# Kernel tuning notes

Measured on AMD Instinct MI355X. Metric: run time of the kernel, lower is better.

Reference implementation:

```python
import jax, jax.numpy as jnp
import numpy as np

DISTANCE_SCALE = 25.0
VIEW_PE = 6
STEP = 0.02  # nominal ray-march step size used to scale dists


def positional_encoding(positions, freqs):
    # matches torch: (positions[..., None] * 2**k).reshape(..., freqs*C) -> [sin, cos]
    freq_bands = 2.0 ** jnp.arange(freqs, dtype=positions.dtype)
    pts = (positions[..., None] * freq_bands).reshape(positions.shape[:-1] + (freqs * positions.shape[-1],))
    return jnp.concatenate([jnp.sin(pts), jnp.cos(pts)], axis=-1)


def setup_inputs() -> dict:
    key = jax.random.key(0)
    ks = jax.random.split(key, 10)
    n_rays, n_samples, C, featureC = 4096, 256, 27, 128
    in_mlpC = 3 + 2 * VIEW_PE * 3 + C  # 66
    density_features = jax.random.normal(ks[0], (n_rays, n_samples), jnp.float32)
    app_features = jax.random.normal(ks[1], (n_rays, n_samples, C), jnp.float32)
    viewdirs = jax.random.normal(ks[2], (n_rays, 3), jnp.float32)
    viewdirs = viewdirs / jnp.linalg.norm(viewdirs, axis=-1, keepdims=True)
    dists = jax.random.uniform(ks[3], (n_rays, n_samples), jnp.float32) * STEP
    s1 = 1.0 / np.sqrt(in_mlpC)
    s2 = 1.0 / np.sqrt(featureC)
    W1 = jax.random.uniform(ks[4], (in_mlpC, featureC), jnp.float32, -s1, s1)
    b1 = jax.random.uniform(ks[5], (featureC,), jnp.float32, -s1, s1)
    W2 = jax.random.uniform(ks[6], (featureC, featureC), jnp.float32, -s2, s2)
    b2 = jax.random.uniform(ks[7], (featureC,), jnp.float32, -s2, s2)
    W3 = jax.random.uniform(ks[8], (featureC, 3), jnp.float32, -s2, s2)
    b3 = jnp.zeros((3,), jnp.float32)  # torch init: constant_(bias, 0)
    return {"density_features": density_features, "app_features": app_features,
            "viewdirs": viewdirs, "dists": dists,
            "W1": W1, "b1": b1, "W2": W2, "b2": b2, "W3": W3, "b3": b3}


def reference(density_features, app_features, viewdirs, dists, W1, b1, W2, b2, W3, b3):
    # feature2density (relu activation)
    sigma = jax.nn.relu(density_features)  # [R, S]
    # raw2alpha
    alpha = 1.0 - jnp.exp(-sigma * dists * DISTANCE_SCALE)  # [R, S]
    T = jnp.cumprod(jnp.concatenate([jnp.ones((alpha.shape[0], 1), alpha.dtype),
                                     1.0 - alpha + 1e-10], axis=-1), axis=-1)
    weights = alpha * T[:, :-1]  # [R, S]
    # radiance MLP over all sample points
    R, S, C = app_features.shape
    vd = jnp.broadcast_to(viewdirs[:, None, :], (R, S, 3))
    mlp_in = jnp.concatenate([app_features, vd, positional_encoding(vd, VIEW_PE)], axis=-1)  # [R,S,66]
    h = jax.nn.relu(mlp_in @ W1 + b1)
    h = jax.nn.relu(h @ W2 + b2)
    rgb = jax.nn.sigmoid(h @ W3 + b3)  # [R, S, 3]
    # composite (white background)
    acc_map = jnp.sum(weights, axis=-1)  # [R]
    rgb_map = jnp.einsum('rs,rsc->rc', weights, rgb)  # [R, 3]
    rgb_map = jnp.clip(rgb_map + (1.0 - acc_map[:, None]), 0.0, 1.0)
    return rgb_map
```

## Files before the change

### kernel.cpp

```cpp
#include <hip/hip_runtime.h>
#include <hip/hip_bf16.h>

typedef float f32x4 __attribute__((ext_vector_type(4)));
typedef short s16x8 __attribute__((ext_vector_type(8)));
typedef unsigned int u32;
typedef u32 u32x2 __attribute__((ext_vector_type(2)));

#define DIST_SCALE 25.0f

__device__ __forceinline__ unsigned short f2b(float f) {
  union { float f; unsigned u; } v; v.f = f;
  unsigned r = v.u + 0x7fffu + ((v.u >> 16) & 1u);
  return (unsigned short)(r >> 16);
}

__device__ __forceinline__ u32 cvtpk(float lo, float hi) {
  u32 r;
  asm("v_cvt_pk_bf16_f32 %0, %1, %2" : "=v"(r) : "v"(lo), "v"(hi));
  return r;
}

__device__ __forceinline__ int swzH(int s, int chbyte) {
  return (s * 256 + chbyte) ^ ((s & 7) << 4);
}

__global__ void prep_weights(const float* __restrict__ W1, const float* __restrict__ W2,
                             const float* __restrict__ W3, unsigned short* __restrict__ ws) {
  int t = blockIdx.x * 256 + threadIdx.x;
  int stride = gridDim.x * 256;
  for (int i = t; i < 128 * 32; i += stride) {
    int n = i >> 5, k = i & 31;
    ws[i] = (k < 27) ? f2b(W1[k * 128 + n]) : (unsigned short)0;
  }
  unsigned short* w2t = ws + 4096;
  for (int i = t; i < 128 * 128; i += stride) {
    int n = i >> 7, k = i & 127;
    w2t[i] = f2b(W2[k * 128 + n]);
  }
  unsigned short* w3p = ws + 4096 + 16384;
  for (int i = t; i < 4 * 16 * 32; i += stride) {
    int wv = i >> 9, rem = i & 511, n = rem >> 5, ks = rem & 31;
    int kg = ks >> 3, j = ks & 7;
    int ch = wv * 32 + ((j >> 2) << 4) + kg * 4 + (j & 3);
    w3p[i] = (n < 3) ? f2b(W3[ch * 3 + n]) : (unsigned short)0;
  }
}

__global__ void __launch_bounds__(256, 3) nerf_main(
    const float* __restrict__ dens, const float* __restrict__ app,
    const float* __restrict__ vdirs, const float* __restrict__ dists,
    const float* __restrict__ W1, const float* __restrict__ b1,
    const float* __restrict__ b2v, const float* __restrict__ b3v,
    const unsigned short* __restrict__ wsb, float* __restrict__ out) {
  __shared__ unsigned short HA[64 * 128];
  __shared__ __align__(16) float pool[768];
  __shared__ float wbuf[256];
  __shared__ float red[4][4];

  const int t = threadIdx.x;
  const int lane = t & 63;
  const int wv = t >> 6;
  const int r = blockIdx.x;

  const unsigned short* W1aT = wsb;
  const unsigned short* W2T = wsb + 4096;
  const unsigned short* W3P = wsb + 4096 + 16384;
  char* HAb = (char*)HA;

  const int cl = lane & 15;
  const int kg = lane >> 4;
  const int chBase = wv * 32;
  float* featbuf = pool;
  float* hcbuf = pool + 64;

  if (t < 39) {
    float val;
    if (t < 3) val = vdirs[r * 3 + t];
    else {
      int jj = t - 3;
      int trig = jj / 18;
      int rem = jj % 18;
      int c = rem / 6, k = rem % 6;
      float v = vdirs[r * 3 + c] * (float)(1 << k);
      val = trig ? cosf(v) : sinf(v);
    }
    featbuf[t] = val;
  }
  if (wv == 0) {
    const float4 dv = *(const float4*)(dens + (size_t)r * 256 + lane * 4);
    const float4 tv = *(const float4*)(dists + (size_t)r * 256 + lane * 4);
    float f[4], al[4];
    float dl[4] = {dv.x, dv.y, dv.z, dv.w};
    float tl[4] = {tv.x, tv.y, tv.z, tv.w};
    float p = 1.0f;
#pragma unroll
    for (int q = 0; q < 4; ++q) {
      float sg = fmaxf(dl[q], 0.0f);
      float e = __expf(-sg * tl[q] * DIST_SCALE);
      al[q] = 1.0f - e;
      f[q] = e + 1e-10f;
      p *= f[q];
    }
    float P = p;
#pragma unroll
    for (int dlt = 1; dlt < 64; dlt <<= 1) {
      float v = __shfl_up(P, dlt, 64);
      if (lane >= dlt) P *= v;
    }
    float E = __shfl_up(P, 1, 64);
    if (lane == 0) E = 1.0f;
    float tr = E;
#pragma unroll
    for (int q = 0; q < 4; ++q) { wbuf[lane * 4 + q] = al[q] * tr; tr *= f[q]; }
  }
  __syncthreads();
  if (t < 128) {
    float s = b1[t];
    for (int j = 0; j < 39; ++j) s += featbuf[j] * W1[(27 + j) * 128 + t];
    hcbuf[t] = s;
  }

  s16x8 w1f[2], w2f[2][4], w3s;
#pragma unroll
  for (int nt = 0; nt < 2; ++nt)
    w1f[nt] = *(const s16x8*)(W1aT + (chBase + nt * 16 + cl) * 32 + kg * 8);
#pragma unroll
  for (int nt = 0; nt < 2; ++nt)
#pragma unroll
    for (int kk = 0; kk < 4; ++kk)
      w2f[nt][kk] = *(const s16x8*)(W2T + (chBase + nt * 16 + cl) * 128 + kk * 32 + kg * 8);
  w3s = *(const s16x8*)(W3P + wv * 512 + cl * 32 + kg * 8);

  __syncthreads();
  const f32x4 hc0 = *(const f32x4*)(hcbuf + chBase + kg * 4);
  const f32x4 hc1 = *(const f32x4*)(hcbuf + chBase + 16 + kg * 4);
  const f32x4 bb0 = *(const f32x4*)(b2v + chBase + kg * 4);
  const f32x4 bb1 = *(const f32x4*)(b2v + chBase + 16 + kg * 4);
  const float b3c = (kg < 3) ? b3v[kg] : 0.0f;
  float pacc = 0.0f;
  float* part = pool;

  const float* rayBase = app + (size_t)r * 6912;

  for (int chunk = 0; chunk < 4; ++chunk) {
    const int sBase = chunk * 64;
    const float* ckBase = rayBase + chunk * 1728;
    const bool tailCk = (r == 4095) && (chunk == 3);

#pragma unroll
    for (int st = 0; st < 4; ++st) {
      const int s = st * 16 + cl;
      const float* gp = ckBase + s * 27 + kg * 8;
      f32x4 va, vb;
      if (__builtin_expect(tailCk && st == 3, 0)) {
        if (kg == 3 && cl == 15) {
          va = (f32x4){gp[0], gp[1], gp[2], 0.0f};
          vb = (f32x4){0.0f, 0.0f, 0.0f, 0.0f};
        } else {
          va = *(const f32x4*)gp;
          vb = *(const f32x4*)(gp + 4);
        }
      } else {
        va = *(const f32x4*)gp;
        vb = *(const f32x4*)(gp + 4);
      }
      union { u32 u[4]; s16x8 v; } xb;
      xb.u[0] = cvtpk(va[0], va[1]);
      xb.u[1] = cvtpk(va[2], va[3]);
      xb.u[2] = cvtpk(vb[0], vb[1]);
      xb.u[3] = cvtpk(vb[2], vb[3]);
      f32x4 a0 = hc0, a1 = hc1;
      a0 = __builtin_amdgcn_mfma_f32_16x16x32_bf16(w1f[0], xb.v, a0, 0, 0, 0);
      a1 = __builtin_amdgcn_mfma_f32_16x16x32_bf16(w1f[1], xb.v, a1, 0, 0, 0);
      u32x2 pk0 = {cvtpk(fmaxf(a0[0], 0.0f), fmaxf(a0[1], 0.0f)),
                   cvtpk(fmaxf(a0[2], 0.0f), fmaxf(a0[3], 0.0f))};
      u32x2 pk1 = {cvtpk(fmaxf(a1[0], 0.0f), fmaxf(a1[1], 0.0f)),
                   cvtpk(fmaxf(a1[2], 0.0f), fmaxf(a1[3], 0.0f))};
      *(u32x2*)(HAb + swzH(s, (chBase + kg * 4) * 2)) = pk0;
      *(u32x2*)(HAb + swzH(s, (chBase + 16 + kg * 4) * 2)) = pk1;
    }
    __syncthreads();

#pragma unroll
    for (int st = 0; st < 4; ++st) {
      const int s = st * 16 + cl;
      s16x8 hbf[4];
#pragma unroll
      for (int kk = 0; kk < 4; ++kk)
        hbf[kk] = *(const s16x8*)(HAb + swzH(s, (kk * 32 + kg * 8) * 2));
      f32x4 a0 = bb0, a1 = bb1;
#pragma unroll
      for (int kk = 0; kk < 4; ++kk) {
        a0 = __builtin_amdgcn_mfma_f32_16x16x32_bf16(w2f[0][kk], hbf[kk], a0, 0, 0, 0);
        a1 = __builtin_amdgcn_mfma_f32_16x16x32_bf16(w2f[1][kk], hbf[kk], a1, 0, 0, 0);
      }
      union { u32 u[4]; s16x8 v; } b3;
      b3.u[0] = cvtpk(fmaxf(a0[0], 0.0f), fmaxf(a0[1], 0.0f));
      b3.u[1] = cvtpk(fmaxf(a0[2], 0.0f), fmaxf(a0[3], 0.0f));
      b3.u[2] = cvtpk(fmaxf(a1[0], 0.0f), fmaxf(a1[1], 0.0f));
      b3.u[3] = cvtpk(fmaxf(a1[2], 0.0f), fmaxf(a1[3], 0.0f));
      f32x4 p3 = {};
      p3 = __builtin_amdgcn_mfma_f32_16x16x32_bf16(w3s, b3.v, p3, 0, 0, 0);
      if (kg == 0) {
        float* pp = part + s * 12;
        pp[wv] = p3[0];
        pp[4 + wv] = p3[1];
        pp[8 + wv] = p3[2];
      }
    }
    __syncthreads();

    {
      const int s = wv * 16 + cl;
      const float w = wbuf[sBase + s];
      if (kg < 3) {
        f32x4 pv = *(const f32x4*)(part + s * 12 + kg * 4);
        float v = (pv[0] + pv[1]) + (pv[2] + pv[3]) + b3c;
        pacc += w / (1.0f + __expf(-v));
      } else {
        pacc += w;
      }
    }
  }

#pragma unroll
  for (int d = 1; d < 16; d <<= 1) pacc += __shfl_xor(pacc, d, 64);
  if (cl == 0) red[wv][kg] = pacc;
  __syncthreads();
  if (t == 0) {
    float R = red[0][0] + red[1][0] + red[2][0] + red[3][0];
    float G = red[0][1] + red[1][1] + red[2][1] + red[3][1];
    float B = red[0][2] + red[1][2] + red[2][2] + red[3][2];
    float W = red[0][3] + red[1][3] + red[2][3] + red[3][3];
    float bg = 1.0f - W;
    out[r * 3 + 0] = fminf(fmaxf(R + bg, 0.0f), 1.0f);
    out[r * 3 + 1] = fminf(fmaxf(G + bg, 0.0f), 1.0f);
    out[r * 3 + 2] = fminf(fmaxf(B + bg, 0.0f), 1.0f);
  }
}

extern "C" void kernel_launch(void* const* d_in, const int* in_sizes, int n_in,
                              void* d_out, int out_size, void* d_ws, size_t ws_size,
                              hipStream_t stream) {
  const float* dens = (const float*)d_in[0];
  const float* app  = (const float*)d_in[1];
  const float* vd   = (const float*)d_in[2];
  const float* dist = (const float*)d_in[3];
  const float* W1   = (const float*)d_in[4];
  const float* b1   = (const float*)d_in[5];
  const float* W2   = (const float*)d_in[6];
  const float* b2   = (const float*)d_in[7];
  const float* W3   = (const float*)d_in[8];
  const float* b3   = (const float*)d_in[9];
  unsigned short* wsb = (unsigned short*)d_ws;

  prep_weights<<<32, 256, 0, stream>>>(W1, W2, W3, wsb);
  nerf_main<<<4096, 256, 0, stream>>>(dens, app, vd, dist, W1, b1, b2, b3, wsb, (float*)d_out);
}
```

Measured before the change: 94.34 us.

## Double-buffer hidden activations and prefetch next chunk's features per wave

Layer 1 is reorganized so each wave computes all 128 hidden channels for its own 16 samples, using all eight W1 fragments, instead of a 32-channel slice across all 64 samples. The HA and partial-output buffers are double-buffered, which removes one barrier per chunk. The next chunk's app features are prefetched into registers while the current chunk is processed. The cost is higher register pressure from the extra W1 fragments and from dropping the occupancy hint in launch_bounds, plus doubled shared memory.

```diff
diff --git a/kernel.cpp b/kernel.cpp
--- a/kernel.cpp
+++ b/kernel.cpp
@@ -46,15 +46,17 @@
   }
 }
 
-__global__ void __launch_bounds__(256, 3) nerf_main(
+__global__ void __launch_bounds__(256) nerf_main(
     const float* __restrict__ dens, const float* __restrict__ app,
     const float* __restrict__ vdirs, const float* __restrict__ dists,
     const float* __restrict__ W1, const float* __restrict__ b1,
     const float* __restrict__ b2v, const float* __restrict__ b3v,
     const unsigned short* __restrict__ wsb, float* __restrict__ out) {
-  __shared__ unsigned short HA[64 * 128];
-  __shared__ __align__(16) float pool[768];
+  __shared__ unsigned short HA[2][64 * 128];
+  __shared__ __align__(16) float part[2][64 * 12];
   __shared__ float wbuf[256];
+  __shared__ float hcbuf[128];
+  __shared__ float featbuf[40];
   __shared__ float red[4][4];
 
   const int t = threadIdx.x;
@@ -65,13 +67,20 @@
   const unsigned short* W1aT = wsb;
   const unsigned short* W2T = wsb + 4096;
   const unsigned short* W3P = wsb + 4096 + 16384;
-  char* HAb = (char*)HA;
 
   const int cl = lane & 15;
   const int kg = lane >> 4;
   const int chBase = wv * 32;
-  float* featbuf = pool;
-  float* hcbuf = pool + 64;
+  const int myS = wv * 16 + cl;
+
+  const float* rayBase = app + (size_t)r * 6912;
+
+  f32x4 va, vb;
+  {
+    const float* gp = rayBase + myS * 27 + kg * 8;
+    va = *(const f32x4*)gp;
+    vb = *(const f32x4*)(gp + 4);
+  }
 
   if (t < 39) {
     float val;
@@ -120,10 +129,10 @@
     hcbuf[t] = s;
   }
 
-  s16x8 w1f[2], w2f[2][4], w3s;
-#pragma unroll
-  for (int nt = 0; nt < 2; ++nt)
-    w1f[nt] = *(const s16x8*)(W1aT + (chBase + nt * 16 + cl) * 32 + kg * 8);
+  s16x8 w1f[8], w2f[2][4], w3s;
+#pragma unroll
+  for (int nt = 0; nt < 8; ++nt)
+    w1f[nt] = *(const s16x8*)(W1aT + (nt * 16 + cl) * 32 + kg * 8);
 #pragma unroll
   for (int nt = 0; nt < 2; ++nt)
 #pragma unroll
@@ -131,55 +140,57 @@
       w2f[nt][kk] = *(const s16x8*)(W2T + (chBase + nt * 16 + cl) * 128 + kk * 32 + kg * 8);
   w3s = *(const s16x8*)(W3P + wv * 512 + cl * 32 + kg * 8);
 
-  __syncthreads();
-  const f32x4 hc0 = *(const f32x4*)(hcbuf + chBase + kg * 4);
-  const f32x4 hc1 = *(const f32x4*)(hcbuf + chBase + 16 + kg * 4);
   const f32x4 bb0 = *(const f32x4*)(b2v + chBase + kg * 4);
   const f32x4 bb1 = *(const f32x4*)(b2v + chBase + 16 + kg * 4);
+  const float b30 = b3v[0], b31 = b3v[1], b32 = b3v[2];
   const float b3c = (kg < 3) ? b3v[kg] : 0.0f;
   float pacc = 0.0f;
-  float* part = pool;
-
-  const float* rayBase = app + (size_t)r * 6912;
+
+  __syncthreads();
 
   for (int chunk = 0; chunk < 4; ++chunk) {
-    const int sBase = chunk * 64;
-    const float* ckBase = rayBase + chunk * 1728;
-    const bool tailCk = (r == 4095) && (chunk == 3);
-
-#pragma unroll
-    for (int st = 0; st < 4; ++st) {
-      const int s = st * 16 + cl;
-      const float* gp = ckBase + s * 27 + kg * 8;
-      f32x4 va, vb;
-      if (__builtin_expect(tailCk && st == 3, 0)) {
-        if (kg == 3 && cl == 15) {
-          va = (f32x4){gp[0], gp[1], gp[2], 0.0f};
-          vb = (f32x4){0.0f, 0.0f, 0.0f, 0.0f};
-        } else {
-          va = *(const f32x4*)gp;
-          vb = *(const f32x4*)(gp + 4);
-        }
-      } else {
-        va = *(const f32x4*)gp;
-        vb = *(const f32x4*)(gp + 4);
-      }
+    char* HAc = (char*)HA[chunk & 1];
+
+    {
       union { u32 u[4]; s16x8 v; } xb;
       xb.u[0] = cvtpk(va[0], va[1]);
       xb.u[1] = cvtpk(va[2], va[3]);
       xb.u[2] = cvtpk(vb[0], vb[1]);
       xb.u[3] = cvtpk(vb[2], vb[3]);
-      f32x4 a0 = hc0, a1 = hc1;
-      a0 = __builtin_amdgcn_mfma_f32_16x16x32_bf16(w1f[0], xb.v, a0, 0, 0, 0);
-      a1 = __builtin_amdgcn_mfma_f32_16x16x32_bf16(w1f[1], xb.v, a1, 0, 0, 0);
-      u32x2 pk0 = {cvtpk(fmaxf(a0[0], 0.0f), fmaxf(a0[1], 0.0f)),
-                   cvtpk(fmaxf(a0[2], 0.0f), fmaxf(a0[3], 0.0f))};
-      u32x2 pk1 = {cvtpk(fmaxf(a1[0], 0.0f), fmaxf(a1[1], 0.0f)),
-                   cvtpk(fmaxf(a1[2], 0.0f), fmaxf(a1[3], 0.0f))};
-      *(u32x2*)(HAb + swzH(s, (chBase + kg * 4) * 2)) = pk0;
-      *(u32x2*)(HAb + swzH(s, (chBase + 16 + kg * 4) * 2)) = pk1;
-    }
+#pragma unroll
+      for (int nt = 0; nt < 8; ++nt) {
+        f32x4 hcf = *(const f32x4*)(hcbuf + nt * 16 + kg * 4);
+        f32x4 a = hcf;
+        a = __builtin_amdgcn_mfma_f32_16x16x32_bf16(w1f[nt], xb.v, a, 0, 0, 0);
+        u32x2 pk = {cvtpk(fmaxf(a[0], 0.0f), fmaxf(a[1], 0.0f)),
+                    cvtpk(fmaxf(a[2], 0.0f), fmaxf(a[3], 0.0f))};
+        *(u32x2*)(HAc + swzH(myS, (nt * 16 + kg * 4) * 2)) = pk;
+      }
+    }
+
+    if (chunk < 3) {
+      const float* gp = rayBase + (chunk + 1) * 1728 + myS * 27 + kg * 8;
+      if (__builtin_expect(r == 4095 && chunk == 2 && myS == 63 && kg == 3, 0)) {
+        va = (f32x4){gp[0], gp[1], gp[2], 0.0f};
+        vb = (f32x4){0.0f, 0.0f, 0.0f, 0.0f};
+      } else {
+        va = *(const f32x4*)gp;
+        vb = *(const f32x4*)(gp + 4);
+      }
+    }
+
     __syncthreads();
+
+    if (chunk > 0) {
+      const float w = wbuf[(chunk - 1) * 64 + myS];
+      if (kg < 3) {
+        f32x4 pv = *(const f32x4*)(part[(chunk - 1) & 1] + myS * 12 + kg * 4);
+        float v = (pv[0] + pv[1]) + (pv[2] + pv[3]) + b3c;
+        pacc += w / (1.0f + __expf(-v));
+      } else {
+        pacc += w;
+      }
+    }
 
 #pragma unroll
     for (int st = 0; st < 4; ++st) {
@@ -187,7 +198,7 @@
       s16x8 hbf[4];
 #pragma unroll
       for (int kk = 0; kk < 4; ++kk)
-        hbf[kk] = *(const s16x8*)(HAb + swzH(s, (kk * 32 + kg * 8) * 2));
+        hbf[kk] = *(const s16x8*)(HAc + swzH(s, (kk * 32 + kg * 8) * 2));
       f32x4 a0 = bb0, a1 = bb1;
 #pragma unroll
       for (int kk = 0; kk < 4; ++kk) {
@@ -202,27 +213,25 @@
       f32x4 p3 = {};
       p3 = __builtin_amdgcn_mfma_f32_16x16x32_bf16(w3s, b3.v, p3, 0, 0, 0);
       if (kg == 0) {
-        float* pp = part + s * 12;
+        float* pp = part[chunk & 1] + s * 12;
         pp[wv] = p3[0];
         pp[4 + wv] = p3[1];
         pp[8 + wv] = p3[2];
       }
     }
-    __syncthreads();
-
-    {
-      const int s = wv * 16 + cl;
-      const float w = wbuf[sBase + s];
-      if (kg < 3) {
-        f32x4 pv = *(const f32x4*)(part + s * 12 + kg * 4);
-        float v = (pv[0] + pv[1]) + (pv[2] + pv[3]) + b3c;
-        pacc += w / (1.0f + __expf(-v));
-      } else {
-        pacc += w;
-      }
-    }
-  }
-
+  }
+
+  __syncthreads();
+  {
+    const float w = wbuf[3 * 64 + myS];
+    if (kg < 3) {
+      f32x4 pv = *(const f32x4*)(part[1] + myS * 12 + kg * 4);
+      float v = (pv[0] + pv[1]) + (pv[2] + pv[3]) + b3c;
+      pacc += w / (1.0f + __expf(-v));
+    } else {
+      pacc += w;
+    }
+  }
 #pragma unroll
   for (int d = 1; d < 16; d <<= 1) pacc += __shfl_xor(pacc, d, 64);
   if (cl == 0) red[wv][kg] = pacc;
```

After: 77.50 us. 17.9% less time.
